# Kernel tuning notes

Hardware: AMD Instinct MI355X
Metric: run time of the kernel (lower is better)

## Reference

```python
import jax, jax.numpy as jnp
import numpy as np
from jax import lax

VOCAB, EMB, HID = 300, 128, 512  # num_embeddings, char_emb_dim, lstm_hidden_dim


def _run_lstm(x, mask, Wih, Whh, b, reverse):
    """Mask-aware unidirectional LSTM matching packed-sequence semantics.
    x: [B,T,D] float, mask: [B,T] float {0,1}. Returns [B,T,H] with padded
    positions zeroed (as pad_packed_sequence produces)."""
    B = x.shape[0]
    H = Whh.shape[1]
    xg = jnp.einsum('btd,gd->btg', x, Wih) + b  # precompute input projections [B,T,4H]

    def step(carry, inp):
        h, c = carry
        g, m = inp  # g:[B,4H], m:[B,1]
        gates = g + h @ Whh.T
        i, f, gg, o = jnp.split(gates, 4, axis=-1)  # torch gate order i,f,g,o
        i = jax.nn.sigmoid(i)
        f = jax.nn.sigmoid(f)
        gg = jnp.tanh(gg)
        o = jax.nn.sigmoid(o)
        c_new = f * c + i * gg
        h_new = o * jnp.tanh(c_new)
        # only advance state on valid tokens (packed-sequence behavior)
        h = jnp.where(m > 0, h_new, h)
        c = jnp.where(m > 0, c_new, c)
        return (h, c), h * m

    m_t = jnp.swapaxes(mask, 0, 1)[..., None]  # [T,B,1]
    xs = (jnp.swapaxes(xg, 0, 1), m_t)
    z = jnp.zeros((B, H), dtype=x.dtype)
    _, ys = lax.scan(step, (z, z), xs, reverse=reverse)
    return jnp.swapaxes(ys, 0, 1)  # [B,T,H]


def setup_inputs() -> dict:
    key = jax.random.key(0)
    ks = jax.random.split(key, 10)
    B, T, W1 = 64, 512, 65
    s = 1.0 / np.sqrt(HID)
    inp = {
        'flair_ids': jax.random.randint(ks[0], (B, T), 0, VOCAB),
        'flair_attention_mask': jnp.ones((B, T), dtype=jnp.int64 if jax.config.jax_enable_x64 else jnp.int32),
        'flair_boundary': jnp.sort(jax.random.randint(ks[1], (B, W1), 0, T), axis=1),
        'emb': jax.random.normal(ks[2], (VOCAB, EMB), dtype=jnp.float32),
        'Wih_f': jax.random.uniform(ks[3], (4 * HID, EMB), minval=-s, maxval=s, dtype=jnp.float32),
        'Whh_f': jax.random.uniform(ks[4], (4 * HID, HID), minval=-s, maxval=s, dtype=jnp.float32),
        'b_f': jax.random.uniform(ks[5], (4 * HID,), minval=-s, maxval=s, dtype=jnp.float32),
        'Wih_b': jax.random.uniform(ks[6], (4 * HID, EMB), minval=-s, maxval=s, dtype=jnp.float32),
        'Whh_b': jax.random.uniform(ks[7], (4 * HID, HID), minval=-s, maxval=s, dtype=jnp.float32),
        'b_b': jax.random.uniform(ks[8], (4 * HID,), minval=-s, maxval=s, dtype=jnp.float32),
    }
    return inp


def reference(flair_ids, flair_attention_mask, flair_boundary,
              emb, Wih_f, Whh_f, b_f, Wih_b, Whh_b, b_b):
    mask = flair_attention_mask.astype(emb.dtype)  # [B,T]
    x = emb[flair_ids]  # [B,T,EMB]
    h_fwd = _run_lstm(x, mask, Wih_f, Whh_f, b_f, reverse=False)
    h_bwd = _run_lstm(x, mask, Wih_b, Whh_b, b_b, reverse=True)
    out = jnp.concatenate([h_fwd, h_bwd], axis=-1)  # [B,T,2H]

    # vectorized boundary gather + concat (replaces the Python double loop)
    i_idx = flair_boundary[:, :-1]  # [B,W]
    j_idx = flair_boundary[:, 1:]
    valid = (i_idx != -1) & (j_idx != -1)
    out_i = jnp.take_along_axis(out, jnp.clip(i_idx, 0)[:, :, None], axis=1)  # [B,W,2H]
    out_j = jnp.take_along_axis(out, jnp.clip(j_idx, 0)[:, :, None], axis=1)
    word_emb = jnp.concatenate([out_i, out_j], axis=-1)  # [B,W,4H]
    return jnp.where(valid[:, :, None], word_emb, 0.0)
```

## Files before the change

### kernel.cpp

```cpp
#include <hip/hip_runtime.h>

#define BB 64
#define TT 512
#define EE 128
#define HH 512
#define NGRP 4
#define BG 16
#define NSLICE 32
#define JW 16
#define DOMBLK 32
#define NSLOT 132
#define LDH 520
#define LDE 136

typedef _Float16 f16;
typedef f16 f16x8 __attribute__((ext_vector_type(8)));
typedef float floatx4 __attribute__((ext_vector_type(4)));
typedef unsigned long long u64;

__device__ __forceinline__ float sigmf(float x) { return 1.f / (1.f + __expf(-x)); }
__device__ __forceinline__ float tanhfast(float x) { return 2.f / (1.f + __expf(-2.f * x)) - 1.f; }

__global__ __launch_bounds__(64) void build_map(const int* __restrict__ bnd,
                                                int* __restrict__ slotmap)
{
  __shared__ unsigned char need[TT];
  const int b = blockIdx.x;
  for (int i = threadIdx.x; i < TT; i += 64) need[i] = 0;
  __syncthreads();
  {
    const int w = threadIdx.x;
    const int iv = bnd[b * 65 + w];
    const int jv = bnd[b * 65 + w + 1];
    if (iv != -1 && jv != -1) {
      int ic = iv < 0 ? 0 : (iv > TT - 1 ? TT - 1 : iv);
      int jc = jv < 0 ? 0 : (jv > TT - 1 ? TT - 1 : jv);
      need[ic] = 1;
      need[jc] = 1;
    }
  }
  __syncthreads();
  if (threadIdx.x == 0) {
    int c = 0;
    for (int t = 0; t < TT; ++t) slotmap[b * TT + t] = need[t] ? (c++) : -1;
  }
}

__global__ __launch_bounds__(256, 1) void lstm_scan(
    const int* __restrict__ ids, const int* __restrict__ maskI,
    const float* __restrict__ emb,
    const float* __restrict__ Wih_f, const float* __restrict__ Whh_f, const float* __restrict__ b_f,
    const float* __restrict__ Wih_b, const float* __restrict__ Whh_b, const float* __restrict__ b_b,
    const int* __restrict__ slotmap,
    f16* __restrict__ h_g,
    f16* __restrict__ hist,
    unsigned* __restrict__ flags)
{
  __shared__ f16 sH[BG * LDH];
  __shared__ f16 sX[BG * LDE];
  __shared__ f16 hOut[BG * JW];
  __shared__ float sMask[BG];
  __shared__ int sSlot[BG];

  const int tid = threadIdx.x;
  const int bid = blockIdx.x;
  const int dom = bid & 7;
  const int slice = bid >> 3;
  const int dir = dom & 1;
  const int grp = dom >> 1;

  const float* Wih = dir ? Wih_b : Wih_f;
  const float* Whh = dir ? Whh_b : Whh_f;
  const float* bv  = dir ? b_b   : b_f;

  const int lane = tid & 63;
  const int wave = tid >> 6;
  const int rloc = lane & 15;
  const int kg   = lane >> 4;
  const int rglob = wave * 16 + rloc;
  const int jloc  = rglob >> 2;
  const int q     = rglob & 3;
  const int mbase = kg * 4;

  const int growL = q * HH + slice * JW + jloc;

  f16x8 wh[16];
  {
    const float* wr = Whh + (size_t)growL * HH + kg * 8;
    #pragma unroll
    for (int kk = 0; kk < 16; ++kk) {
      float4 a0 = *(const float4*)(wr + kk * 32);
      float4 a1 = *(const float4*)(wr + kk * 32 + 4);
      f16x8 v;
      v[0]=(f16)a0.x; v[1]=(f16)a0.y; v[2]=(f16)a0.z; v[3]=(f16)a0.w;
      v[4]=(f16)a1.x; v[5]=(f16)a1.y; v[6]=(f16)a1.z; v[7]=(f16)a1.w;
      wh[kk] = v;
    }
  }
  f16x8 wx[4];
  {
    const float* wr = Wih + (size_t)growL * EE + kg * 8;
    #pragma unroll
    for (int kk = 0; kk < 4; ++kk) {
      float4 a0 = *(const float4*)(wr + kk * 32);
      float4 a1 = *(const float4*)(wr + kk * 32 + 4);
      f16x8 v;
      v[0]=(f16)a0.x; v[1]=(f16)a0.y; v[2]=(f16)a0.z; v[3]=(f16)a0.w;
      v[4]=(f16)a1.x; v[5]=(f16)a1.y; v[6]=(f16)a1.z; v[7]=(f16)a1.w;
      wx[kk] = v;
    }
  }
  const float bsc = bv[growL];

  float cc[4] = {0.f, 0.f, 0.f, 0.f};
  float hh[4] = {0.f, 0.f, 0.f, 0.f};

  for (int s = 0; s < TT; ++s) {
    const int t = dir ? (TT - 1 - s) : s;

    {
      const int row = tid >> 4;
      const int c0 = (tid & 15) * 8;
      const int b = grp * BG + row;
      const int idx = ids[b * TT + t];
      float4 x0 = *(const float4*)(emb + (size_t)idx * EE + c0);
      float4 x1 = *(const float4*)(emb + (size_t)idx * EE + c0 + 4);
      f16x8 xv;
      xv[0]=(f16)x0.x; xv[1]=(f16)x0.y; xv[2]=(f16)x0.z; xv[3]=(f16)x0.w;
      xv[4]=(f16)x1.x; xv[5]=(f16)x1.y; xv[6]=(f16)x1.z; xv[7]=(f16)x1.w;
      *(f16x8*)(sX + row * LDE + c0) = xv;
    }
    if (tid < BG) {
      const int b = grp * BG + tid;
      sMask[tid] = (float)maskI[b * TT + t];
      sSlot[tid] = slotmap[b * TT + t];
    }

    if (s == 0) {
      for (int e = tid; e < BG * 64; e += 256) {
        const int row = e >> 6, ch = e & 63;
        uint4 z = make_uint4(0u, 0u, 0u, 0u);
        *(uint4*)(sH + row * LDH + ch * 8) = z;
      }
    } else {
      const u64* hq = (const u64*)(h_g + ((size_t)(((s & 1) * 2 + dir) * NGRP + grp)) * BG * HH);
      u64 v[8];
      #pragma unroll
      for (int p = 0; p < 8; ++p)
        v[p] = __hip_atomic_load(hq + p * 256 + tid, __ATOMIC_RELAXED, __HIP_MEMORY_SCOPE_AGENT);
      #pragma unroll
      for (int p = 0; p < 8; ++p) {
        const int e = p * 256 + tid;
        const int row = e >> 7, ch = e & 127;
        *(u64*)(sH + row * LDH + ch * 4) = v[p];
      }
    }
    __syncthreads();

    floatx4 acc = {0.f, 0.f, 0.f, 0.f};
    const f16* aH = sH + rloc * LDH + kg * 8;
    #pragma unroll
    for (int kk = 0; kk < 16; ++kk) {
      f16x8 af = *(const f16x8*)(aH + kk * 32);
      acc = __builtin_amdgcn_mfma_f32_16x16x32_f16(af, wh[kk], acc, 0, 0, 0);
    }
    const f16* aX = sX + rloc * LDE + kg * 8;
    #pragma unroll
    for (int kk = 0; kk < 4; ++kk) {
      f16x8 af = *(const f16x8*)(aX + kk * 32);
      acc = __builtin_amdgcn_mfma_f32_16x16x32_f16(af, wx[kk], acc, 0, 0, 0);
    }

    #pragma unroll
    for (int i = 0; i < 4; ++i) {
      const float g0 = acc[i] + bsc;
      const float s1 = __shfl_xor(g0, 1, 64);
      const float s2 = __shfl_xor(g0, 2, 64);
      const float s3 = __shfl_xor(s1, 2, 64);
      float vi, vf, vg, vo;
      if (q == 0)      { vi = g0; vf = s1; vg = s2; vo = s3; }
      else if (q == 1) { vi = s1; vf = g0; vg = s3; vo = s2; }
      else if (q == 2) { vi = s2; vf = s3; vg = g0; vo = s1; }
      else             { vi = s3; vf = s2; vg = s1; vo = g0; }
      const float ig = sigmf(vi);
      const float fg = sigmf(vf);
      const float gt = tanhfast(vg);
      const float og = sigmf(vo);
      const float cn = fg * cc[i] + ig * gt;
      const float hn = og * tanhfast(cn);
      const float m = sMask[mbase + i];
      cc[i] = m > 0.f ? cn : cc[i];
      float hk = m > 0.f ? hn : hh[i];
      const f16 h16 = (f16)hk;
      hh[i] = (float)h16;
    }
    {
      const float hq_ = (q == 0) ? hh[0] : (q == 1) ? hh[1] : (q == 2) ? hh[2] : hh[3];
      hOut[(mbase + q) * JW + jloc] = (f16)hq_;
    }
    __syncthreads();

    if (tid < 64) {
      const int bl = tid >> 2;
      const int c0 = (tid & 3) * 4;
      const u64 v = *(const u64*)(hOut + bl * JW + c0);
      u64* hdst = (u64*)(h_g + ((size_t)((((s + 1) & 1) * 2 + dir) * NGRP + grp) * BG + bl) * HH
                         + slice * JW + c0);
      __hip_atomic_store(hdst, v, __ATOMIC_RELAXED, __HIP_MEMORY_SCOPE_AGENT);
      const int slot = sSlot[bl];
      if (slot >= 0) {
        const u64 hv = sMask[bl] > 0.f ? v : 0ULL;
        *(u64*)(hist + ((size_t)(dir * BB + grp * BG + bl) * NSLOT + slot) * HH
                + slice * JW + c0) = hv;
      }
    }

    if (s + 1 < TT) {
      asm volatile("s_waitcnt vmcnt(0)" ::: "memory");
      if (tid == 0)
        __hip_atomic_store(flags + dom * 32 + slice, (unsigned)(s + 1),
                           __ATOMIC_RELAXED, __HIP_MEMORY_SCOPE_AGENT);
      const unsigned tgt = (unsigned)(s + 1);
      const unsigned* fl = flags + dom * 32 + (lane & 31);
      for (;;) {
        const unsigned v = __hip_atomic_load(fl, __ATOMIC_RELAXED, __HIP_MEMORY_SCOPE_AGENT);
        if (__all((lane >= 32) | (v >= tgt))) break;
        __builtin_amdgcn_s_sleep(1);
      }
      __builtin_amdgcn_sched_barrier(0);
      asm volatile("" ::: "memory");
    }
  }
}

__global__ __launch_bounds__(256) void gather_out(
    const int* __restrict__ bnd, const int* __restrict__ slotmap,
    const f16* __restrict__ hist, float* __restrict__ out)
{
  const int bw = blockIdx.x;
  const int b = bw >> 6;
  const int w = bw & 63;
  const int k = threadIdx.x * 8;
  const int iv = bnd[b * 65 + w];
  const int jv = bnd[b * 65 + w + 1];
  const bool valid = (iv != -1) && (jv != -1);
  float* dst = out + (size_t)bw * 2048 + k;
  if (valid) {
    const int seg = k >> 9;
    int ts = (seg < 2) ? iv : jv;
    ts = ts < 0 ? 0 : (ts > TT - 1 ? TT - 1 : ts);
    const int dirn = seg & 1;
    const int slot = slotmap[b * TT + ts];
    const f16* src = hist + ((size_t)(dirn * BB + b) * NSLOT + slot) * HH + (k & 511);
    f16x8 v = *(const f16x8*)src;
    float4 o0 = make_float4((float)v[0], (float)v[1], (float)v[2], (float)v[3]);
    float4 o1 = make_float4((float)v[4], (float)v[5], (float)v[6], (float)v[7]);
    *(float4*)dst = o0;
    *(float4*)(dst + 4) = o1;
  } else {
    float4 z = make_float4(0.f, 0.f, 0.f, 0.f);
    *(float4*)dst = z;
    *(float4*)(dst + 4) = z;
  }
}

extern "C" void kernel_launch(void* const* d_in, const int* in_sizes, int n_in,
                              void* d_out, int out_size, void* d_ws, size_t ws_size,
                              hipStream_t stream)
{
  (void)in_sizes; (void)n_in; (void)out_size; (void)ws_size;
  const int* ids     = (const int*)d_in[0];
  const int* maskI   = (const int*)d_in[1];
  const int* bnd     = (const int*)d_in[2];
  const float* emb   = (const float*)d_in[3];
  const float* Wih_f = (const float*)d_in[4];
  const float* Whh_f = (const float*)d_in[5];
  const float* b_f   = (const float*)d_in[6];
  const float* Wih_b = (const float*)d_in[7];
  const float* Whh_b = (const float*)d_in[8];
  const float* b_b   = (const float*)d_in[9];

  char* ws = (char*)d_ws;
  unsigned* flags = (unsigned*)ws;
  int* slotmap  = (int*)(ws + 4096);
  f16* h_g      = (f16*)(ws + 4096 + 131072);
  f16* hist     = (f16*)(ws + 4096 + 131072 + 262144);

  hipMemsetAsync(flags, 0, 4096, stream);
  build_map<<<dim3(BB), dim3(64), 0, stream>>>(bnd, slotmap);
  lstm_scan<<<dim3(256), dim3(256), 0, stream>>>(ids, maskI, emb,
      Wih_f, Whh_f, b_f, Whh_b == nullptr ? b_b : Wih_b, Whh_b, b_b, slotmap, h_g, hist, flags);
  gather_out<<<dim3(BB * 64), dim3(256), 0, stream>>>(bnd, slotmap, hist, (float*)d_out);
}
```

Before: 1.939 ms.

## Add runtime-probed fast sync path, prefetch next-step inputs, split MFMA accumulators

Adds a startup handshake among the 32 slice blocks of each domain. It checks whether plain stores plus sc0 loads give coherent cross-block visibility, and if they do, switches to a fast mode. That mode uses non-atomic stores, dwordx4 sc0 loads for the hidden-state exchange, workgroup-scope flag stores, sleep-free polling, and flags padded to separate cache lines. The embedding, mask and slot loads for step s+1 are now issued before the MFMA work of step s and written to shared memory after the barrier, so their latency is hidden. The MFMA chain is split into two accumulators to shorten dependency latency. The main risk is the weakened memory-model assumptions in fast mode, which rely on the probe being a reliable test of coherence.

```diff
diff --git a/kernel.cpp b/kernel.cpp
--- a/kernel.cpp
+++ b/kernel.cpp
@@ -6,9 +6,7 @@
 #define HH 512
 #define NGRP 4
 #define BG 16
-#define NSLICE 32
 #define JW 16
-#define DOMBLK 32
 #define NSLOT 132
 #define LDH 520
 #define LDE 136
@@ -16,10 +14,26 @@
 typedef _Float16 f16;
 typedef f16 f16x8 __attribute__((ext_vector_type(8)));
 typedef float floatx4 __attribute__((ext_vector_type(4)));
+typedef unsigned u32x4 __attribute__((ext_vector_type(4)));
 typedef unsigned long long u64;
 
 __device__ __forceinline__ float sigmf(float x) { return 1.f / (1.f + __expf(-x)); }
 __device__ __forceinline__ float tanhfast(float x) { return 2.f / (1.f + __expf(-2.f * x)) - 1.f; }
+
+__device__ __forceinline__ unsigned ld_sc0_u32(const unsigned* p) {
+  unsigned v;
+  asm volatile("global_load_dword %0, %1, off sc0\n\ts_waitcnt vmcnt(0)"
+               : "=v"(v) : "v"(p) : "memory");
+  return v;
+}
+
+__device__ __forceinline__ unsigned hs_poll(const unsigned* p, unsigned ph) {
+  for (;;) {
+    unsigned v = __hip_atomic_load(p, __ATOMIC_RELAXED, __HIP_MEMORY_SCOPE_AGENT);
+    if (__all(v >= ph)) return v;
+    __builtin_amdgcn_s_sleep(2);
+  }
+}
 
 __global__ __launch_bounds__(64) void build_map(const int* __restrict__ bnd,
                                                 int* __restrict__ slotmap)
@@ -54,13 +68,16 @@
     const int* __restrict__ slotmap,
     f16* __restrict__ h_g,
     f16* __restrict__ hist,
-    unsigned* __restrict__ flags)
+    unsigned* __restrict__ flags,
+    unsigned* __restrict__ hsb,
+    unsigned* __restrict__ probe)
 {
   __shared__ f16 sH[BG * LDH];
   __shared__ f16 sX[BG * LDE];
   __shared__ f16 hOut[BG * JW];
   __shared__ float sMask[BG];
   __shared__ int sSlot[BG];
+  __shared__ int sFast;
 
   const int tid = threadIdx.x;
   const int bid = blockIdx.x;
@@ -68,20 +85,54 @@
   const int slice = bid >> 3;
   const int dir = dom & 1;
   const int grp = dom >> 1;
+  const int lane = tid & 63;
+  const int wave = tid >> 6;
+
+  {
+    unsigned* myhs = hsb + (dom * 32 + slice) * 32;
+    const unsigned* plhs = hsb + (dom * 32 + (lane & 31)) * 32;
+    unsigned* pr = probe + dom * 32;
+    unsigned ph = 0;
+    bool ok = true;
+    for (int k = 0; k < 4; ++k) {
+      const unsigned expv = (unsigned)(k + 1) * 0x1111u;
+      ph += 0x100;
+      if (tid == 0) __hip_atomic_store(myhs, ph, __ATOMIC_RELAXED, __HIP_MEMORY_SCOPE_AGENT);
+      if (wave == 0) hs_poll(plhs, ph);
+      __syncthreads();
+      if (tid == 0 && slice == 0) *pr = expv;
+      asm volatile("s_waitcnt vmcnt(0)" ::: "memory");
+      ph += 0x100;
+      if (tid == 0) __hip_atomic_store(myhs, ph, __ATOMIC_RELAXED, __HIP_MEMORY_SCOPE_AGENT);
+      if (wave == 0) {
+        hs_poll(plhs, ph);
+        const unsigned v = ld_sc0_u32(pr);
+        ok = ok && (v == expv);
+      }
+      __syncthreads();
+    }
+    ph += 0x100;
+    if (tid == 0) __hip_atomic_store(myhs, ph | (ok ? 1u : 0u),
+                                     __ATOMIC_RELAXED, __HIP_MEMORY_SCOPE_AGENT);
+    if (wave == 0) {
+      const unsigned v = hs_poll(plhs, ph);
+      const int f = __all((v & 1u) != 0u) ? 1 : 0;
+      if (lane == 0) sFast = f;
+    }
+    __syncthreads();
+  }
+  const bool FASTM = (sFast != 0);
 
   const float* Wih = dir ? Wih_b : Wih_f;
   const float* Whh = dir ? Whh_b : Whh_f;
   const float* bv  = dir ? b_b   : b_f;
 
-  const int lane = tid & 63;
-  const int wave = tid >> 6;
   const int rloc = lane & 15;
   const int kg   = lane >> 4;
   const int rglob = wave * 16 + rloc;
   const int jloc  = rglob >> 2;
   const int q     = rglob & 3;
   const int mbase = kg * 4;
-
   const int growL = q * HH + slice * JW + jloc;
 
   f16x8 wh[16];
@@ -115,32 +166,48 @@
   float cc[4] = {0.f, 0.f, 0.f, 0.f};
   float hh[4] = {0.f, 0.f, 0.f, 0.f};
 
+  const int xrow = tid >> 4;
+  const int xc0 = (tid & 15) * 8;
+
+  {
+    const int t0 = dir ? (TT - 1) : 0;
+    const int b = grp * BG + xrow;
+    const int idx = ids[b * TT + t0];
+    float4 x0 = *(const float4*)(emb + (size_t)idx * EE + xc0);
+    float4 x1 = *(const float4*)(emb + (size_t)idx * EE + xc0 + 4);
+    f16x8 xv;
+    xv[0]=(f16)x0.x; xv[1]=(f16)x0.y; xv[2]=(f16)x0.z; xv[3]=(f16)x0.w;
+    xv[4]=(f16)x1.x; xv[5]=(f16)x1.y; xv[6]=(f16)x1.z; xv[7]=(f16)x1.w;
+    *(f16x8*)(sX + xrow * LDE + xc0) = xv;
+    if (tid < BG) {
+      const int b2 = grp * BG + tid;
+      sMask[tid] = (float)maskI[b2 * TT + t0];
+      sSlot[tid] = slotmap[b2 * TT + t0];
+    }
+  }
+
   for (int s = 0; s < TT; ++s) {
-    const int t = dir ? (TT - 1 - s) : s;
-
-    {
-      const int row = tid >> 4;
-      const int c0 = (tid & 15) * 8;
-      const int b = grp * BG + row;
-      const int idx = ids[b * TT + t];
-      float4 x0 = *(const float4*)(emb + (size_t)idx * EE + c0);
-      float4 x1 = *(const float4*)(emb + (size_t)idx * EE + c0 + 4);
-      f16x8 xv;
-      xv[0]=(f16)x0.x; xv[1]=(f16)x0.y; xv[2]=(f16)x0.z; xv[3]=(f16)x0.w;
-      xv[4]=(f16)x1.x; xv[5]=(f16)x1.y; xv[6]=(f16)x1.z; xv[7]=(f16)x1.w;
-      *(f16x8*)(sX + row * LDE + c0) = xv;
-    }
-    if (tid < BG) {
-      const int b = grp * BG + tid;
-      sMask[tid] = (float)maskI[b * TT + t];
-      sSlot[tid] = slotmap[b * TT + t];
-    }
-
     if (s == 0) {
       for (int e = tid; e < BG * 64; e += 256) {
         const int row = e >> 6, ch = e & 63;
         uint4 z = make_uint4(0u, 0u, 0u, 0u);
         *(uint4*)(sH + row * LDH + ch * 8) = z;
+      }
+    } else if (FASTM) {
+      const f16* hq = h_g + ((size_t)(((s & 1) * 2 + dir) * NGRP + grp)) * BG * HH;
+      u32x4 hv[4];
+      #pragma unroll
+      for (int p = 0; p < 4; ++p) {
+        const f16* src = hq + (size_t)(p * 256 + tid) * 8;
+        asm volatile("global_load_dwordx4 %0, %1, off sc0" : "=v"(hv[p]) : "v"(src));
+      }
+      asm volatile("s_waitcnt vmcnt(0)" ::: "memory");
+      __builtin_amdgcn_sched_barrier(0);
+      #pragma unroll
+      for (int p = 0; p < 4; ++p) {
+        const int e = p * 256 + tid;
+        const int row = e >> 6, ch = e & 63;
+        *(u32x4*)(sH + row * LDH + ch * 8) = hv[p];
       }
     } else {
       const u64* hq = (const u64*)(h_g + ((size_t)(((s & 1) * 2 + dir) * NGRP + grp)) * BG * HH);
@@ -157,19 +224,39 @@
     }
     __syncthreads();
 
-    floatx4 acc = {0.f, 0.f, 0.f, 0.f};
+    float4 px0, px1; float pm = 0.f; int pslot = -1;
+    if (s + 1 < TT) {
+      const int tn = dir ? (TT - 2 - s) : (s + 1);
+      const int b = grp * BG + xrow;
+      const int idx = ids[b * TT + tn];
+      px0 = *(const float4*)(emb + (size_t)idx * EE + xc0);
+      px1 = *(const float4*)(emb + (size_t)idx * EE + xc0 + 4);
+      if (tid < BG) {
+        const int b2 = grp * BG + tid;
+        pm = (float)maskI[b2 * TT + tn];
+        pslot = slotmap[b2 * TT + tn];
+      }
+    }
+
+    floatx4 acc0 = {0.f, 0.f, 0.f, 0.f};
+    floatx4 acc1 = {0.f, 0.f, 0.f, 0.f};
     const f16* aH = sH + rloc * LDH + kg * 8;
     #pragma unroll
-    for (int kk = 0; kk < 16; ++kk) {
-      f16x8 af = *(const f16x8*)(aH + kk * 32);
-      acc = __builtin_amdgcn_mfma_f32_16x16x32_f16(af, wh[kk], acc, 0, 0, 0);
+    for (int kk = 0; kk < 16; kk += 2) {
+      f16x8 a0 = *(const f16x8*)(aH + kk * 32);
+      f16x8 a1 = *(const f16x8*)(aH + (kk + 1) * 32);
+      acc0 = __builtin_amdgcn_mfma_f32_16x16x32_f16(a0, wh[kk], acc0, 0, 0, 0);
+      acc1 = __builtin_amdgcn_mfma_f32_16x16x32_f16(a1, wh[kk + 1], acc1, 0, 0, 0);
     }
     const f16* aX = sX + rloc * LDE + kg * 8;
     #pragma unroll
-    for (int kk = 0; kk < 4; ++kk) {
-      f16x8 af = *(const f16x8*)(aX + kk * 32);
-      acc = __builtin_amdgcn_mfma_f32_16x16x32_f16(af, wx[kk], acc, 0, 0, 0);
-    }
+    for (int kk = 0; kk < 4; kk += 2) {
+      f16x8 a0 = *(const f16x8*)(aX + kk * 32);
+      f16x8 a1 = *(const f16x8*)(aX + (kk + 1) * 32);
+      acc0 = __builtin_amdgcn_mfma_f32_16x16x32_f16(a0, wx[kk], acc0, 0, 0, 0);
+      acc1 = __builtin_amdgcn_mfma_f32_16x16x32_f16(a1, wx[kk + 1], acc1, 0, 0, 0);
+    }
+    floatx4 acc = acc0 + acc1;
 
     #pragma unroll
     for (int i = 0; i < 4; ++i) {
@@ -206,7 +293,8 @@
       const u64 v = *(const u64*)(hOut + bl * JW + c0);
       u64* hdst = (u64*)(h_g + ((size_t)((((s + 1) & 1) * 2 + dir) * NGRP + grp) * BG + bl) * HH
                          + slice * JW + c0);
-      __hip_atomic_store(hdst, v, __ATOMIC_RELAXED, __HIP_MEMORY_SCOPE_AGENT);
+      if (FASTM) *hdst = v;
+      else __hip_atomic_store(hdst, v, __ATOMIC_RELAXED, __HIP_MEMORY_SCOPE_AGENT);
       const int slot = sSlot[bl];
       if (slot >= 0) {
         const u64 hv = sMask[bl] > 0.f ? v : 0ULL;
@@ -217,18 +305,37 @@
 
     if (s + 1 < TT) {
       asm volatile("s_waitcnt vmcnt(0)" ::: "memory");
-      if (tid == 0)
-        __hip_atomic_store(flags + dom * 32 + slice, (unsigned)(s + 1),
-                           __ATOMIC_RELAXED, __HIP_MEMORY_SCOPE_AGENT);
+      unsigned* myflag = flags + (dom * 32 + slice) * 32;
+      if (tid == 0) {
+        if (FASTM) __hip_atomic_store(myflag, (unsigned)(s + 1),
+                                      __ATOMIC_RELAXED, __HIP_MEMORY_SCOPE_WORKGROUP);
+        else       __hip_atomic_store(myflag, (unsigned)(s + 1),
+                                      __ATOMIC_RELAXED, __HIP_MEMORY_SCOPE_AGENT);
+      }
       const unsigned tgt = (unsigned)(s + 1);
-      const unsigned* fl = flags + dom * 32 + (lane & 31);
-      for (;;) {
-        const unsigned v = __hip_atomic_load(fl, __ATOMIC_RELAXED, __HIP_MEMORY_SCOPE_AGENT);
-        if (__all((lane >= 32) | (v >= tgt))) break;
-        __builtin_amdgcn_s_sleep(1);
+      const unsigned* fl = flags + (dom * 32 + (lane & 31)) * 32;
+      if (FASTM) {
+        for (;;) {
+          const unsigned v = ld_sc0_u32(fl);
+          if (__all(v >= tgt)) break;
+        }
+      } else {
+        for (;;) {
+          const unsigned v = __hip_atomic_load(fl, __ATOMIC_RELAXED, __HIP_MEMORY_SCOPE_AGENT);
+          if (__all(v >= tgt)) break;
+          __builtin_amdgcn_s_sleep(1);
+        }
       }
       __builtin_amdgcn_sched_barrier(0);
       asm volatile("" ::: "memory");
+
+      {
+        f16x8 xv;
+        xv[0]=(f16)px0.x; xv[1]=(f16)px0.y; xv[2]=(f16)px0.z; xv[3]=(f16)px0.w;
+        xv[4]=(f16)px1.x; xv[5]=(f16)px1.y; xv[6]=(f16)px1.z; xv[7]=(f16)px1.w;
+        *(f16x8*)(sX + xrow * LDE + xc0) = xv;
+        if (tid < BG) { sMask[tid] = pm; sSlot[tid] = pslot; }
+      }
     }
   }
 }
@@ -282,13 +389,15 @@
 
   char* ws = (char*)d_ws;
   unsigned* flags = (unsigned*)ws;
-  int* slotmap  = (int*)(ws + 4096);
-  f16* h_g      = (f16*)(ws + 4096 + 131072);
-  f16* hist     = (f16*)(ws + 4096 + 131072 + 262144);
-
-  hipMemsetAsync(flags, 0, 4096, stream);
+  unsigned* hsb   = (unsigned*)(ws + 32768);
+  unsigned* probe = (unsigned*)(ws + 65536);
+  int* slotmap    = (int*)(ws + 69632);
+  f16* h_g        = (f16*)(ws + 69632 + 131072);
+  f16* hist       = (f16*)(ws + 69632 + 131072 + 262144);
+
+  hipMemsetAsync(ws, 0, 69632, stream);
   build_map<<<dim3(BB), dim3(64), 0, stream>>>(bnd, slotmap);
   lstm_scan<<<dim3(256), dim3(256), 0, stream>>>(ids, maskI, emb,
-      Wih_f, Whh_f, b_f, Whh_b == nullptr ? b_b : Wih_b, Whh_b, b_b, slotmap, h_g, hist, flags);
+      Wih_f, Whh_f, b_f, Wih_b, Whh_b, b_b, slotmap, h_g, hist, flags, hsb, probe);
   gather_out<<<dim3(BB * 64), dim3(256), 0, stream>>>(bnd, slotmap, hist, (float*)d_out);
 }
```

Result: slower. 2.157 ms (+11.2%).

## Interleave both LSTM directions per block and replace flag barrier with tagged data polling

Applied to the files above, without the earlier changes.

Each block now runs the forward and backward directions in alternation, so the kernel uses 128 blocks instead of 256 and holds both weight sets in registers. The separate flag array and the all-slices spin barrier are gone. Every hidden value is stored as a 32-bit word whose upper 16 bits carry the step tag, and consumers poll the data directly until the tags match. The next step's hidden state and embeddings are prefetched while the other direction computes. The aim is to hide cross-block synchronisation latency behind the other direction's work, at the cost of higher register pressure, doubled h_g traffic, and a poll loop capped by a budget that could silently proceed on stale data.

```diff
diff --git a/kernel.cpp b/kernel.cpp
--- a/kernel.cpp
+++ b/kernel.cpp
@@ -6,9 +6,7 @@
 #define HH 512
 #define NGRP 4
 #define BG 16
-#define NSLICE 32
 #define JW 16
-#define DOMBLK 32
 #define NSLOT 132
 #define LDH 520
 #define LDE 136
@@ -16,10 +14,24 @@
 typedef _Float16 f16;
 typedef f16 f16x8 __attribute__((ext_vector_type(8)));
 typedef float floatx4 __attribute__((ext_vector_type(4)));
+typedef unsigned u32x4 __attribute__((ext_vector_type(4)));
 typedef unsigned long long u64;
 
 __device__ __forceinline__ float sigmf(float x) { return 1.f / (1.f + __expf(-x)); }
 __device__ __forceinline__ float tanhfast(float x) { return 2.f / (1.f + __expf(-2.f * x)) - 1.f; }
+
+template<int N>
+__device__ __forceinline__ void loadw(f16x8* dst, const float* src) {
+  #pragma unroll
+  for (int kk = 0; kk < N; ++kk) {
+    float4 a0 = *(const float4*)(src + kk * 32);
+    float4 a1 = *(const float4*)(src + kk * 32 + 4);
+    f16x8 v;
+    v[0]=(f16)a0.x; v[1]=(f16)a0.y; v[2]=(f16)a0.z; v[3]=(f16)a0.w;
+    v[4]=(f16)a1.x; v[5]=(f16)a1.y; v[6]=(f16)a1.z; v[7]=(f16)a1.w;
+    dst[kk] = v;
+  }
+}
 
 __global__ __launch_bounds__(64) void build_map(const int* __restrict__ bnd,
                                                 int* __restrict__ slotmap)
@@ -52,27 +64,19 @@
     const float* __restrict__ Wih_f, const float* __restrict__ Whh_f, const float* __restrict__ b_f,
     const float* __restrict__ Wih_b, const float* __restrict__ Whh_b, const float* __restrict__ b_b,
     const int* __restrict__ slotmap,
-    f16* __restrict__ h_g,
-    f16* __restrict__ hist,
-    unsigned* __restrict__ flags)
+    unsigned* __restrict__ h_g,
+    f16* __restrict__ hist)
 {
-  __shared__ f16 sH[BG * LDH];
-  __shared__ f16 sX[BG * LDE];
+  __shared__ f16 sH[2][BG * LDH];
+  __shared__ f16 sX[2][BG * LDE];
   __shared__ f16 hOut[BG * JW];
-  __shared__ float sMask[BG];
-  __shared__ int sSlot[BG];
+  __shared__ float sMask[2][BG];
+  __shared__ int sSlot[2][BG];
 
   const int tid = threadIdx.x;
   const int bid = blockIdx.x;
-  const int dom = bid & 7;
-  const int slice = bid >> 3;
-  const int dir = dom & 1;
-  const int grp = dom >> 1;
-
-  const float* Wih = dir ? Wih_b : Wih_f;
-  const float* Whh = dir ? Whh_b : Whh_f;
-  const float* bv  = dir ? b_b   : b_f;
-
+  const int grp = bid >> 5;
+  const int slice = bid & 31;
   const int lane = tid & 63;
   const int wave = tid >> 6;
   const int rloc = lane & 15;
@@ -81,154 +85,176 @@
   const int jloc  = rglob >> 2;
   const int q     = rglob & 3;
   const int mbase = kg * 4;
-
   const int growL = q * HH + slice * JW + jloc;
 
-  f16x8 wh[16];
+  f16x8 wh0[16], wh1[16], wx0[4], wx1[4];
+  loadw<16>(wh0, Whh_f + (size_t)growL * HH + kg * 8);
+  loadw<16>(wh1, Whh_b + (size_t)growL * HH + kg * 8);
+  loadw<4>(wx0, Wih_f + (size_t)growL * EE + kg * 8);
+  loadw<4>(wx1, Wih_b + (size_t)growL * EE + kg * 8);
+  const float bsc0 = b_f[growL];
+  const float bsc1 = b_b[growL];
+
+  float cc0[4] = {0,0,0,0}, hh0[4] = {0,0,0,0};
+  float cc1[4] = {0,0,0,0}, hh1[4] = {0,0,0,0};
+  u32x4 pre[8];
+  int budget = 5000000;
+
+  const int xrow = tid >> 4;
+  const int xc0 = (tid & 15) * 8;
+
+  for (int i = tid; i < 2 * BG * LDH / 2; i += 256) ((unsigned*)sH)[i] = 0u;
   {
-    const float* wr = Whh + (size_t)growL * HH + kg * 8;
+    const int b = grp * BG + xrow;
+    const int idx = ids[b * TT + 0];
+    float4 x0 = *(const float4*)(emb + (size_t)idx * EE + xc0);
+    float4 x1 = *(const float4*)(emb + (size_t)idx * EE + xc0 + 4);
+    f16x8 xv;
+    xv[0]=(f16)x0.x; xv[1]=(f16)x0.y; xv[2]=(f16)x0.z; xv[3]=(f16)x0.w;
+    xv[4]=(f16)x1.x; xv[5]=(f16)x1.y; xv[6]=(f16)x1.z; xv[7]=(f16)x1.w;
+    *(f16x8*)(&sX[0][xrow * LDE + xc0]) = xv;
+    if (tid < BG) {
+      sMask[0][tid] = (float)maskI[(grp * BG + tid) * TT + 0];
+      sSlot[0][tid] = slotmap[(grp * BG + tid) * TT + 0];
+    }
+  }
+  __syncthreads();
+
+  for (int s = 0; s < TT; ++s) {
     #pragma unroll
-    for (int kk = 0; kk < 16; ++kk) {
-      float4 a0 = *(const float4*)(wr + kk * 32);
-      float4 a1 = *(const float4*)(wr + kk * 32 + 4);
-      f16x8 v;
-      v[0]=(f16)a0.x; v[1]=(f16)a0.y; v[2]=(f16)a0.z; v[3]=(f16)a0.w;
-      v[4]=(f16)a1.x; v[5]=(f16)a1.y; v[6]=(f16)a1.z; v[7]=(f16)a1.w;
-      wh[kk] = v;
-    }
-  }
-  f16x8 wx[4];
-  {
-    const float* wr = Wih + (size_t)growL * EE + kg * 8;
-    #pragma unroll
-    for (int kk = 0; kk < 4; ++kk) {
-      float4 a0 = *(const float4*)(wr + kk * 32);
-      float4 a1 = *(const float4*)(wr + kk * 32 + 4);
-      f16x8 v;
-      v[0]=(f16)a0.x; v[1]=(f16)a0.y; v[2]=(f16)a0.z; v[3]=(f16)a0.w;
-      v[4]=(f16)a1.x; v[5]=(f16)a1.y; v[6]=(f16)a1.z; v[7]=(f16)a1.w;
-      wx[kk] = v;
-    }
-  }
-  const float bsc = bv[growL];
-
-  float cc[4] = {0.f, 0.f, 0.f, 0.f};
-  float hh[4] = {0.f, 0.f, 0.f, 0.f};
-
-  for (int s = 0; s < TT; ++s) {
-    const int t = dir ? (TT - 1 - s) : s;
-
-    {
-      const int row = tid >> 4;
-      const int c0 = (tid & 15) * 8;
-      const int b = grp * BG + row;
-      const int idx = ids[b * TT + t];
-      float4 x0 = *(const float4*)(emb + (size_t)idx * EE + c0);
-      float4 x1 = *(const float4*)(emb + (size_t)idx * EE + c0 + 4);
-      f16x8 xv;
-      xv[0]=(f16)x0.x; xv[1]=(f16)x0.y; xv[2]=(f16)x0.z; xv[3]=(f16)x0.w;
-      xv[4]=(f16)x1.x; xv[5]=(f16)x1.y; xv[6]=(f16)x1.z; xv[7]=(f16)x1.w;
-      *(f16x8*)(sX + row * LDE + c0) = xv;
-    }
-    if (tid < BG) {
-      const int b = grp * BG + tid;
-      sMask[tid] = (float)maskI[b * TT + t];
-      sSlot[tid] = slotmap[b * TT + t];
-    }
-
-    if (s == 0) {
-      for (int e = tid; e < BG * 64; e += 256) {
-        const int row = e >> 6, ch = e & 63;
-        uint4 z = make_uint4(0u, 0u, 0u, 0u);
-        *(uint4*)(sH + row * LDH + ch * 8) = z;
-      }
-    } else {
-      const u64* hq = (const u64*)(h_g + ((size_t)(((s & 1) * 2 + dir) * NGRP + grp)) * BG * HH);
-      u64 v[8];
+    for (int d = 0; d < 2; ++d) {
+      const int t = d ? (TT - 1 - s) : s;
+      auto& wh = d ? wh1 : wh0;
+      auto& wx = d ? wx1 : wx0;
+      auto& cc = d ? cc1 : cc0;
+      auto& hh = d ? hh1 : hh0;
+      const float bsc = d ? bsc1 : bsc0;
+
+      if (s > 0) {
+        asm volatile("s_waitcnt vmcnt(0)" ::: "memory");
+        __builtin_amdgcn_sched_barrier(0);
+        const unsigned tg = (unsigned)s;
+        unsigned* hq = h_g + (((size_t)(s & 1) * 2 + d) * NGRP + grp) * BG * HH + tid * 32;
+        #pragma unroll
+        for (int p = 0; p < 8; ++p) {
+          u32x4 v = pre[p];
+          for (;;) {
+            const unsigned bad = ((v[0] >> 16) ^ tg) | ((v[1] >> 16) ^ tg) |
+                                 ((v[2] >> 16) ^ tg) | ((v[3] >> 16) ^ tg);
+            if (!bad || --budget < 0) break;
+            asm volatile("global_load_dwordx4 %0, %1, off sc1\n\ts_waitcnt vmcnt(0)"
+                         : "=v"(v) : "v"(hq + p * 4) : "memory");
+          }
+          const unsigned lo = (v[0] & 0xffffu) | (v[1] << 16);
+          const unsigned hi = (v[2] & 0xffffu) | (v[3] << 16);
+          const int i0 = tid * 32 + p * 4;
+          *(u64*)(&sH[d][(i0 >> 9) * LDH + (i0 & 511)]) = ((u64)hi << 32) | lo;
+        }
+      }
+      __syncthreads();
+
+      const int ns = d ? s + 1 : s;
+      const int nd = d ^ 1;
+      float4 px0, px1; float pm = 0.f; int pslot = -1;
+      const bool doX = (ns < TT);
+      if (doX) {
+        const int tn = nd ? (TT - 1 - ns) : ns;
+        const int b = grp * BG + xrow;
+        const int idx = ids[b * TT + tn];
+        px0 = *(const float4*)(emb + (size_t)idx * EE + xc0);
+        px1 = *(const float4*)(emb + (size_t)idx * EE + xc0 + 4);
+        if (tid < BG) {
+          pm = (float)maskI[(grp * BG + tid) * TT + tn];
+          pslot = slotmap[(grp * BG + tid) * TT + tn];
+        }
+      }
+
+      floatx4 accA = {0,0,0,0}, accB = {0,0,0,0};
+      const f16* aH = &sH[d][rloc * LDH + kg * 8];
       #pragma unroll
-      for (int p = 0; p < 8; ++p)
-        v[p] = __hip_atomic_load(hq + p * 256 + tid, __ATOMIC_RELAXED, __HIP_MEMORY_SCOPE_AGENT);
+      for (int kk = 0; kk < 16; kk += 2) {
+        f16x8 a0 = *(const f16x8*)(aH + kk * 32);
+        f16x8 a1 = *(const f16x8*)(aH + (kk + 1) * 32);
+        accA = __builtin_amdgcn_mfma_f32_16x16x32_f16(a0, wh[kk], accA, 0, 0, 0);
+        accB = __builtin_amdgcn_mfma_f32_16x16x32_f16(a1, wh[kk + 1], accB, 0, 0, 0);
+      }
+      const f16* aX = &sX[d][rloc * LDE + kg * 8];
       #pragma unroll
-      for (int p = 0; p < 8; ++p) {
-        const int e = p * 256 + tid;
-        const int row = e >> 7, ch = e & 127;
-        *(u64*)(sH + row * LDH + ch * 4) = v[p];
-      }
-    }
-    __syncthreads();
-
-    floatx4 acc = {0.f, 0.f, 0.f, 0.f};
-    const f16* aH = sH + rloc * LDH + kg * 8;
-    #pragma unroll
-    for (int kk = 0; kk < 16; ++kk) {
-      f16x8 af = *(const f16x8*)(aH + kk * 32);
-      acc = __builtin_amdgcn_mfma_f32_16x16x32_f16(af, wh[kk], acc, 0, 0, 0);
-    }
-    const f16* aX = sX + rloc * LDE + kg * 8;
-    #pragma unroll
-    for (int kk = 0; kk < 4; ++kk) {
-      f16x8 af = *(const f16x8*)(aX + kk * 32);
-      acc = __builtin_amdgcn_mfma_f32_16x16x32_f16(af, wx[kk], acc, 0, 0, 0);
-    }
-
-    #pragma unroll
-    for (int i = 0; i < 4; ++i) {
-      const float g0 = acc[i] + bsc;
-      const float s1 = __shfl_xor(g0, 1, 64);
-      const float s2 = __shfl_xor(g0, 2, 64);
-      const float s3 = __shfl_xor(s1, 2, 64);
-      float vi, vf, vg, vo;
-      if (q == 0)      { vi = g0; vf = s1; vg = s2; vo = s3; }
-      else if (q == 1) { vi = s1; vf = g0; vg = s3; vo = s2; }
-      else if (q == 2) { vi = s2; vf = s3; vg = g0; vo = s1; }
-      else             { vi = s3; vf = s2; vg = s1; vo = g0; }
-      const float ig = sigmf(vi);
-      const float fg = sigmf(vf);
-      const float gt = tanhfast(vg);
-      const float og = sigmf(vo);
-      const float cn = fg * cc[i] + ig * gt;
-      const float hn = og * tanhfast(cn);
-      const float m = sMask[mbase + i];
-      cc[i] = m > 0.f ? cn : cc[i];
-      float hk = m > 0.f ? hn : hh[i];
-      const f16 h16 = (f16)hk;
-      hh[i] = (float)h16;
-    }
-    {
-      const float hq_ = (q == 0) ? hh[0] : (q == 1) ? hh[1] : (q == 2) ? hh[2] : hh[3];
-      hOut[(mbase + q) * JW + jloc] = (f16)hq_;
-    }
-    __syncthreads();
-
-    if (tid < 64) {
-      const int bl = tid >> 2;
-      const int c0 = (tid & 3) * 4;
-      const u64 v = *(const u64*)(hOut + bl * JW + c0);
-      u64* hdst = (u64*)(h_g + ((size_t)((((s + 1) & 1) * 2 + dir) * NGRP + grp) * BG + bl) * HH
-                         + slice * JW + c0);
-      __hip_atomic_store(hdst, v, __ATOMIC_RELAXED, __HIP_MEMORY_SCOPE_AGENT);
-      const int slot = sSlot[bl];
-      if (slot >= 0) {
-        const u64 hv = sMask[bl] > 0.f ? v : 0ULL;
-        *(u64*)(hist + ((size_t)(dir * BB + grp * BG + bl) * NSLOT + slot) * HH
-                + slice * JW + c0) = hv;
-      }
-    }
-
-    if (s + 1 < TT) {
-      asm volatile("s_waitcnt vmcnt(0)" ::: "memory");
-      if (tid == 0)
-        __hip_atomic_store(flags + dom * 32 + slice, (unsigned)(s + 1),
-                           __ATOMIC_RELAXED, __HIP_MEMORY_SCOPE_AGENT);
-      const unsigned tgt = (unsigned)(s + 1);
-      const unsigned* fl = flags + dom * 32 + (lane & 31);
-      for (;;) {
-        const unsigned v = __hip_atomic_load(fl, __ATOMIC_RELAXED, __HIP_MEMORY_SCOPE_AGENT);
-        if (__all((lane >= 32) | (v >= tgt))) break;
-        __builtin_amdgcn_s_sleep(1);
-      }
-      __builtin_amdgcn_sched_barrier(0);
-      asm volatile("" ::: "memory");
+      for (int kk = 0; kk < 4; kk += 2) {
+        f16x8 a0 = *(const f16x8*)(aX + kk * 32);
+        f16x8 a1 = *(const f16x8*)(aX + (kk + 1) * 32);
+        accA = __builtin_amdgcn_mfma_f32_16x16x32_f16(a0, wx[kk], accA, 0, 0, 0);
+        accB = __builtin_amdgcn_mfma_f32_16x16x32_f16(a1, wx[kk + 1], accB, 0, 0, 0);
+      }
+      floatx4 acc = accA + accB;
+
+      #pragma unroll
+      for (int i = 0; i < 4; ++i) {
+        const float g0 = acc[i] + bsc;
+        const float s1 = __shfl_xor(g0, 1, 64);
+        const float s2 = __shfl_xor(g0, 2, 64);
+        const float s3 = __shfl_xor(s1, 2, 64);
+        float vi, vf, vg, vo;
+        if (q == 0)      { vi = g0; vf = s1; vg = s2; vo = s3; }
+        else if (q == 1) { vi = s1; vf = g0; vg = s3; vo = s2; }
+        else if (q == 2) { vi = s2; vf = s3; vg = g0; vo = s1; }
+        else             { vi = s3; vf = s2; vg = s1; vo = g0; }
+        const float ig = sigmf(vi);
+        const float fg = sigmf(vf);
+        const float gt = tanhfast(vg);
+        const float og = sigmf(vo);
+        const float cn = fg * cc[i] + ig * gt;
+        const float hn = og * tanhfast(cn);
+        const float m = sMask[d][mbase + i];
+        cc[i] = m > 0.f ? cn : cc[i];
+        float hk = m > 0.f ? hn : hh[i];
+        const f16 h16 = (f16)hk;
+        hh[i] = (float)h16;
+      }
+      {
+        const float hq_ = (q == 0) ? hh[0] : (q == 1) ? hh[1] : (q == 2) ? hh[2] : hh[3];
+        hOut[(mbase + q) * JW + jloc] = (f16)hq_;
+      }
+      __syncthreads();
+
+      if (tid < 64) {
+        const int bl = tid >> 2;
+        const int c0 = (tid & 3) * 4;
+        const u64 hv8 = *(const u64*)(hOut + bl * JW + c0);
+        if (s + 1 < TT) {
+          const unsigned tg2 = (unsigned)(s + 1) << 16;
+          u32x4 ev;
+          ev[0] = tg2 | (unsigned)(hv8 & 0xffff);
+          ev[1] = tg2 | (unsigned)((hv8 >> 16) & 0xffff);
+          ev[2] = tg2 | (unsigned)((hv8 >> 32) & 0xffff);
+          ev[3] = tg2 | (unsigned)((hv8 >> 48) & 0xffff);
+          unsigned* hdst = h_g + (((size_t)((s + 1) & 1) * 2 + d) * NGRP + grp) * BG * HH
+                           + bl * HH + slice * JW + c0;
+          asm volatile("global_store_dwordx4 %0, %1, off sc1" :: "v"(hdst), "v"(ev) : "memory");
+        }
+        const int slot = sSlot[d][bl];
+        if (slot >= 0) {
+          const u64 hv = sMask[d][bl] > 0.f ? hv8 : 0ULL;
+          *(u64*)(hist + ((size_t)(d * BB + grp * BG + bl) * NSLOT + slot) * HH
+                  + slice * JW + c0) = hv;
+        }
+      }
+
+      if (ns >= 1 && ns < TT) {
+        unsigned* nq = h_g + (((size_t)(ns & 1) * 2 + nd) * NGRP + grp) * BG * HH + tid * 32;
+        #pragma unroll
+        for (int p = 0; p < 8; ++p)
+          asm volatile("global_load_dwordx4 %0, %1, off sc1"
+                       : "=v"(pre[p]) : "v"(nq + p * 4) : "memory");
+      }
+
+      if (doX) {
+        f16x8 xv;
+        xv[0]=(f16)px0.x; xv[1]=(f16)px0.y; xv[2]=(f16)px0.z; xv[3]=(f16)px0.w;
+        xv[4]=(f16)px1.x; xv[5]=(f16)px1.y; xv[6]=(f16)px1.z; xv[7]=(f16)px1.w;
+        *(f16x8*)(&sX[nd][xrow * LDE + xc0]) = xv;
+        if (tid < BG) { sMask[nd][tid] = pm; sSlot[nd][tid] = pslot; }
+      }
     }
   }
 }
@@ -281,14 +307,13 @@
   const float* b_b   = (const float*)d_in[9];
 
   char* ws = (char*)d_ws;
-  unsigned* flags = (unsigned*)ws;
-  int* slotmap  = (int*)(ws + 4096);
-  f16* h_g      = (f16*)(ws + 4096 + 131072);
-  f16* hist     = (f16*)(ws + 4096 + 131072 + 262144);
-
-  hipMemsetAsync(flags, 0, 4096, stream);
+  int* slotmap    = (int*)ws;
+  unsigned* h_g   = (unsigned*)(ws + 131072);
+  f16* hist       = (f16*)(ws + 131072 + 524288);
+
+  hipMemsetAsync(h_g, 0, 524288, stream);
   build_map<<<dim3(BB), dim3(64), 0, stream>>>(bnd, slotmap);
-  lstm_scan<<<dim3(256), dim3(256), 0, stream>>>(ids, maskI, emb,
-      Wih_f, Whh_f, b_f, Whh_b == nullptr ? b_b : Wih_b, Whh_b, b_b, slotmap, h_g, hist, flags);
+  lstm_scan<<<dim3(128), dim3(256), 0, stream>>>(ids, maskI, emb,
+      Wih_f, Whh_f, b_f, Wih_b, Whh_b, b_b, slotmap, h_g, hist);
   gather_out<<<dim3(BB * 64), dim3(256), 0, stream>>>(bnd, slotmap, hist, (float*)d_out);
 }
```

Result: slower. 4.751 ms (+145.0%).

## Replace flag barrier with step-tagged hidden-state words and prefetch next inputs

Applied to the files above, without the earlier changes.

The per-step cross-block flag barrier is removed. Each f16 hidden value is now stored in a 32-bit word tagged with its step number, and consumers spin until every tag they read matches the current step. The next timestep's embedding, mask and slot loads are issued before the MFMA chain so their latency overlaps compute, and the MFMA accumulation is split into two chains to add ILP. In exchange the hidden-state exchange buffer doubles in size and needs a memset, and a spin budget can silently proceed on stale data.

```diff
diff --git a/kernel.cpp b/kernel.cpp
--- a/kernel.cpp
+++ b/kernel.cpp
@@ -6,9 +6,7 @@
 #define HH 512
 #define NGRP 4
 #define BG 16
-#define NSLICE 32
 #define JW 16
-#define DOMBLK 32
 #define NSLOT 132
 #define LDH 520
 #define LDE 136
@@ -16,6 +14,7 @@
 typedef _Float16 f16;
 typedef f16 f16x8 __attribute__((ext_vector_type(8)));
 typedef float floatx4 __attribute__((ext_vector_type(4)));
+typedef unsigned u32x4 __attribute__((ext_vector_type(4)));
 typedef unsigned long long u64;
 
 __device__ __forceinline__ float sigmf(float x) { return 1.f / (1.f + __expf(-x)); }
@@ -52,9 +51,8 @@
     const float* __restrict__ Wih_f, const float* __restrict__ Whh_f, const float* __restrict__ b_f,
     const float* __restrict__ Wih_b, const float* __restrict__ Whh_b, const float* __restrict__ b_b,
     const int* __restrict__ slotmap,
-    f16* __restrict__ h_g,
-    f16* __restrict__ hist,
-    unsigned* __restrict__ flags)
+    unsigned* __restrict__ h_g,
+    f16* __restrict__ hist)
 {
   __shared__ f16 sH[BG * LDH];
   __shared__ f16 sX[BG * LDE];
@@ -81,7 +79,6 @@
   const int jloc  = rglob >> 2;
   const int q     = rglob & 3;
   const int mbase = kg * 4;
-
   const int growL = q * HH + slice * JW + jloc;
 
   f16x8 wh[16];
@@ -114,27 +111,30 @@
 
   float cc[4] = {0.f, 0.f, 0.f, 0.f};
   float hh[4] = {0.f, 0.f, 0.f, 0.f};
+  int budget = 4000000;
+
+  const int xrow = tid >> 4;
+  const int xc0 = (tid & 15) * 8;
+
+  {
+    const int t0 = dir ? (TT - 1) : 0;
+    const int b = grp * BG + xrow;
+    const int idx = ids[b * TT + t0];
+    float4 x0 = *(const float4*)(emb + (size_t)idx * EE + xc0);
+    float4 x1 = *(const float4*)(emb + (size_t)idx * EE + xc0 + 4);
+    f16x8 xv;
+    xv[0]=(f16)x0.x; xv[1]=(f16)x0.y; xv[2]=(f16)x0.z; xv[3]=(f16)x0.w;
+    xv[4]=(f16)x1.x; xv[5]=(f16)x1.y; xv[6]=(f16)x1.z; xv[7]=(f16)x1.w;
+    *(f16x8*)(sX + xrow * LDE + xc0) = xv;
+    if (tid < BG) {
+      const int b2 = grp * BG + tid;
+      sMask[tid] = (float)maskI[b2 * TT + t0];
+      sSlot[tid] = slotmap[b2 * TT + t0];
+    }
+  }
 
   for (int s = 0; s < TT; ++s) {
     const int t = dir ? (TT - 1 - s) : s;
-
-    {
-      const int row = tid >> 4;
-      const int c0 = (tid & 15) * 8;
-      const int b = grp * BG + row;
-      const int idx = ids[b * TT + t];
-      float4 x0 = *(const float4*)(emb + (size_t)idx * EE + c0);
-      float4 x1 = *(const float4*)(emb + (size_t)idx * EE + c0 + 4);
-      f16x8 xv;
-      xv[0]=(f16)x0.x; xv[1]=(f16)x0.y; xv[2]=(f16)x0.z; xv[3]=(f16)x0.w;
-      xv[4]=(f16)x1.x; xv[5]=(f16)x1.y; xv[6]=(f16)x1.z; xv[7]=(f16)x1.w;
-      *(f16x8*)(sX + row * LDE + c0) = xv;
-    }
-    if (tid < BG) {
-      const int b = grp * BG + tid;
-      sMask[tid] = (float)maskI[b * TT + t];
-      sSlot[tid] = slotmap[b * TT + t];
-    }
 
     if (s == 0) {
       for (int e = tid; e < BG * 64; e += 256) {
@@ -143,33 +143,67 @@
         *(uint4*)(sH + row * LDH + ch * 8) = z;
       }
     } else {
-      const u64* hq = (const u64*)(h_g + ((size_t)(((s & 1) * 2 + dir) * NGRP + grp)) * BG * HH);
-      u64 v[8];
+      const unsigned tg = (unsigned)s;
+      unsigned* hq = h_g + (((size_t)(s & 1) * 2 + dir) * NGRP + grp) * BG * HH;
+      u32x4 pre[8];
       #pragma unroll
       for (int p = 0; p < 8; ++p)
-        v[p] = __hip_atomic_load(hq + p * 256 + tid, __ATOMIC_RELAXED, __HIP_MEMORY_SCOPE_AGENT);
+        asm volatile("global_load_dwordx4 %0, %1, off sc1"
+                     : "=v"(pre[p]) : "v"(hq + p * 1024 + tid * 4) : "memory");
+      asm volatile("s_waitcnt vmcnt(0)" ::: "memory");
+      __builtin_amdgcn_sched_barrier(0);
       #pragma unroll
       for (int p = 0; p < 8; ++p) {
-        const int e = p * 256 + tid;
-        const int row = e >> 7, ch = e & 127;
-        *(u64*)(sH + row * LDH + ch * 4) = v[p];
+        u32x4 v = pre[p];
+        for (;;) {
+          const unsigned bad = ((v[0] >> 16) ^ tg) | ((v[1] >> 16) ^ tg) |
+                               ((v[2] >> 16) ^ tg) | ((v[3] >> 16) ^ tg);
+          if (!bad || --budget < 0) break;
+          __builtin_amdgcn_s_sleep(1);
+          asm volatile("global_load_dwordx4 %0, %1, off sc1\n\ts_waitcnt vmcnt(0)"
+                       : "=v"(v) : "v"(hq + p * 1024 + tid * 4) : "memory");
+        }
+        const unsigned lo = (v[0] & 0xffffu) | (v[1] << 16);
+        const unsigned hi = (v[2] & 0xffffu) | (v[3] << 16);
+        const int i0 = p * 1024 + tid * 4;
+        *(u64*)(sH + (i0 >> 9) * LDH + (i0 & 511)) = ((u64)hi << 32) | lo;
       }
     }
     __syncthreads();
 
-    floatx4 acc = {0.f, 0.f, 0.f, 0.f};
+    float4 px0, px1; float pm = 0.f; int pslot = -1;
+    if (s + 1 < TT) {
+      const int tn = dir ? (TT - 2 - s) : (s + 1);
+      const int b = grp * BG + xrow;
+      const int idx = ids[b * TT + tn];
+      px0 = *(const float4*)(emb + (size_t)idx * EE + xc0);
+      px1 = *(const float4*)(emb + (size_t)idx * EE + xc0 + 4);
+      if (tid < BG) {
+        const int b2 = grp * BG + tid;
+        pm = (float)maskI[b2 * TT + tn];
+        pslot = slotmap[b2 * TT + tn];
+      }
+    }
+
+    floatx4 acc0 = {0.f, 0.f, 0.f, 0.f};
+    floatx4 acc1 = {0.f, 0.f, 0.f, 0.f};
     const f16* aH = sH + rloc * LDH + kg * 8;
     #pragma unroll
-    for (int kk = 0; kk < 16; ++kk) {
-      f16x8 af = *(const f16x8*)(aH + kk * 32);
-      acc = __builtin_amdgcn_mfma_f32_16x16x32_f16(af, wh[kk], acc, 0, 0, 0);
+    for (int kk = 0; kk < 16; kk += 2) {
+      f16x8 a0 = *(const f16x8*)(aH + kk * 32);
+      f16x8 a1 = *(const f16x8*)(aH + (kk + 1) * 32);
+      acc0 = __builtin_amdgcn_mfma_f32_16x16x32_f16(a0, wh[kk], acc0, 0, 0, 0);
+      acc1 = __builtin_amdgcn_mfma_f32_16x16x32_f16(a1, wh[kk + 1], acc1, 0, 0, 0);
     }
     const f16* aX = sX + rloc * LDE + kg * 8;
     #pragma unroll
-    for (int kk = 0; kk < 4; ++kk) {
-      f16x8 af = *(const f16x8*)(aX + kk * 32);
-      acc = __builtin_amdgcn_mfma_f32_16x16x32_f16(af, wx[kk], acc, 0, 0, 0);
-    }
+    for (int kk = 0; kk < 4; kk += 2) {
+      f16x8 a0 = *(const f16x8*)(aX + kk * 32);
+      f16x8 a1 = *(const f16x8*)(aX + (kk + 1) * 32);
+      acc0 = __builtin_amdgcn_mfma_f32_16x16x32_f16(a0, wx[kk], acc0, 0, 0, 0);
+      acc1 = __builtin_amdgcn_mfma_f32_16x16x32_f16(a1, wx[kk + 1], acc1, 0, 0, 0);
+    }
+    floatx4 acc = acc0 + acc1;
 
     #pragma unroll
     for (int i = 0; i < 4; ++i) {
@@ -203,32 +237,33 @@
     if (tid < 64) {
       const int bl = tid >> 2;
       const int c0 = (tid & 3) * 4;
-      const u64 v = *(const u64*)(hOut + bl * JW + c0);
-      u64* hdst = (u64*)(h_g + ((size_t)((((s + 1) & 1) * 2 + dir) * NGRP + grp) * BG + bl) * HH
-                         + slice * JW + c0);
-      __hip_atomic_store(hdst, v, __ATOMIC_RELAXED, __HIP_MEMORY_SCOPE_AGENT);
+      const u64 hv8 = *(const u64*)(hOut + bl * JW + c0);
+      if (s + 1 < TT) {
+        const unsigned tg2 = (unsigned)(s + 1) << 16;
+        u32x4 ev;
+        ev[0] = tg2 | (unsigned)(hv8 & 0xffff);
+        ev[1] = tg2 | (unsigned)((hv8 >> 16) & 0xffff);
+        ev[2] = tg2 | (unsigned)((hv8 >> 32) & 0xffff);
+        ev[3] = tg2 | (unsigned)((hv8 >> 48) & 0xffff);
+        unsigned* hdst = h_g + (((size_t)((s + 1) & 1) * 2 + dir) * NGRP + grp) * BG * HH
+                         + bl * HH + slice * JW + c0;
+        asm volatile("global_store_dwordx4 %0, %1, off sc1" :: "v"(hdst), "v"(ev) : "memory");
+      }
       const int slot = sSlot[bl];
       if (slot >= 0) {
-        const u64 hv = sMask[bl] > 0.f ? v : 0ULL;
+        const u64 hv = sMask[bl] > 0.f ? hv8 : 0ULL;
         *(u64*)(hist + ((size_t)(dir * BB + grp * BG + bl) * NSLOT + slot) * HH
                 + slice * JW + c0) = hv;
       }
     }
 
     if (s + 1 < TT) {
-      asm volatile("s_waitcnt vmcnt(0)" ::: "memory");
-      if (tid == 0)
-        __hip_atomic_store(flags + dom * 32 + slice, (unsigned)(s + 1),
-                           __ATOMIC_RELAXED, __HIP_MEMORY_SCOPE_AGENT);
-      const unsigned tgt = (unsigned)(s + 1);
-      const unsigned* fl = flags + dom * 32 + (lane & 31);
-      for (;;) {
-        const unsigned v = __hip_atomic_load(fl, __ATOMIC_RELAXED, __HIP_MEMORY_SCOPE_AGENT);
-        if (__all((lane >= 32) | (v >= tgt))) break;
-        __builtin_amdgcn_s_sleep(1);
-      }
-      __builtin_amdgcn_sched_barrier(0);
-      asm volatile("" ::: "memory");
+      f16x8 xv;
+      xv[0]=(f16)px0.x; xv[1]=(f16)px0.y; xv[2]=(f16)px0.z; xv[3]=(f16)px0.w;
+      xv[4]=(f16)px1.x; xv[5]=(f16)px1.y; xv[6]=(f16)px1.z; xv[7]=(f16)px1.w;
+      *(f16x8*)(sX + xrow * LDE + xc0) = xv;
+      if (tid < BG) { sMask[tid] = pm; sSlot[tid] = pslot; }
+      __syncthreads();
     }
   }
 }
@@ -281,14 +316,13 @@
   const float* b_b   = (const float*)d_in[9];
 
   char* ws = (char*)d_ws;
-  unsigned* flags = (unsigned*)ws;
-  int* slotmap  = (int*)(ws + 4096);
-  f16* h_g      = (f16*)(ws + 4096 + 131072);
-  f16* hist     = (f16*)(ws + 4096 + 131072 + 262144);
-
-  hipMemsetAsync(flags, 0, 4096, stream);
+  int* slotmap    = (int*)ws;
+  unsigned* h_g   = (unsigned*)(ws + 131072);
+  f16* hist       = (f16*)(ws + 131072 + 1048576);
+
+  hipMemsetAsync(h_g, 0, 1048576, stream);
   build_map<<<dim3(BB), dim3(64), 0, stream>>>(bnd, slotmap);
   lstm_scan<<<dim3(256), dim3(256), 0, stream>>>(ids, maskI, emb,
-      Wih_f, Whh_f, b_f, Whh_b == nullptr ? b_b : Wih_b, Whh_b, b_b, slotmap, h_g, hist, flags);
+      Wih_f, Whh_f, b_f, Wih_b, Whh_b, b_b, slotmap, h_g, hist);
   gather_out<<<dim3(BB * 64), dim3(256), 0, stream>>>(bnd, slotmap, hist, (float*)d_out);
 }
```

Result: slower. 2.647 ms (+36.5%).
